# Performance work log

Measured on AMD Instinct MI355X. Metric: run time of the kernel, lower is better.

The kernel has to match this reference:

```python
import jax, jax.numpy as jnp
import numpy as np

N = 8192        # nodes (A.shape[0])
D_IN = 128      # input_dim
D_OUT = 128     # output_dim
D_THETA = 256   # hardcoded in GCN_liner_theta_1
DROP_KEEP = 0.8 # DropEdge percent


def setup_inputs() -> dict:
    key = jax.random.key(0)
    ks = jax.random.split(key, 6)
    H = jax.random.normal(ks[0], (N, D_IN), dtype=jnp.float32)
    U = jax.random.uniform(ks[1], (N, N), dtype=jnp.float32)
    upper = jnp.triu((U < 0.01).astype(jnp.float32), 1)
    A_adj = upper + upper.T + jnp.eye(N, dtype=jnp.float32)
    bn_gamma = jnp.ones((D_IN,), jnp.float32)
    bn_beta = jnp.zeros((D_IN,), jnp.float32)
    W_theta = jax.random.normal(ks[2], (D_THETA, D_IN), jnp.float32) * 0.05
    b_theta = jnp.zeros((D_THETA,), jnp.float32)
    W_out = jax.random.normal(ks[3], (D_OUT, D_IN), jnp.float32) * 0.05
    b_out = jnp.zeros((D_OUT,), jnp.float32)
    return {"H": H, "A_adj": A_adj, "bn_gamma": bn_gamma, "bn_beta": bn_beta,
            "W_theta": W_theta, "b_theta": b_theta, "W_out": W_out, "b_out": b_out}


def reference(H, A_adj, bn_gamma, bn_beta, W_theta, b_theta, W_out, b_out):
    n = H.shape[0]
    # BatchNorm1d in training mode: batch stats over the node dimension
    mean = H.mean(axis=0)
    var = H.var(axis=0)  # biased, matches torch training normalization
    Hn = (H - mean) * jax.lax.rsqrt(var + 1e-5) * bn_gamma + bn_beta

    # theta projection -> pairwise euclidean distances
    Hx = Hn @ W_theta.T + b_theta                     # [N, 256]
    sq = jnp.sum(Hx * Hx, axis=1)                     # [N]
    dist = sq[:, None] + sq[None, :] - 2.0 * (Hx @ Hx.T)
    dist = jnp.sqrt(jnp.clip(dist, 1e-12, None))      # [N, N]

    A = jnp.exp(-0.2 * dist)
    A = jnp.clip(jax.nn.sigmoid(A), 0.1, None)
    # DropEdge detaches A in the original (A never carries grad)
    A = jax.lax.stop_gradient(A)

    dkey = jax.random.key(42)
    keep = jax.random.uniform(dkey, (n, n)) < DROP_KEEP
    triu = jnp.triu(jnp.ones((n, n), dtype=bool), 0)
    Bt = jnp.where(triu & keep, A, 0.0)
    B = Bt + Bt.T - jnp.diag(jnp.diag(Bt))

    mask = jnp.ceil(A_adj * 1e-5)
    A2 = B * mask + jnp.eye(n, dtype=B.dtype)
    A3 = jnp.where(A2 > 0.6, A2, 0.0)                 # threshold (host loop in torch)

    # symmetric normalization D^-1/2 A D^-1/2 without dense diag matmuls
    d_inv_sqrt = jax.lax.rsqrt(A3.sum(axis=1))        # diag always >= 1
    A_hat = A3 * d_inv_sqrt[:, None] * d_inv_sqrt[None, :]

    out = A_hat @ (Hn @ W_out.T + b_out)              # [N, D_OUT]
    out = jnp.where(out >= 0, out, 0.01 * out)        # LeakyReLU(0.01)
    return out, A3
```

## Files before the change

kernel.cpp:

```cpp
#include <hip/hip_runtime.h>
#include <cstdint>
#include <cstddef>

#define N 8192
#define DIN 128
#define DTH 256
#define DOUT 128
#define ROWCAP 256
#define LISTCAP 256

typedef float vfloat4 __attribute__((ext_vector_type(4)));

__device__ __forceinline__ void threefry_0_42(uint32_t x0, uint32_t x1,
                                              uint32_t& o0, uint32_t& o1) {
  const uint32_t ks0 = 0u;
  const uint32_t ks1 = 42u;
  const uint32_t ks2 = 0x1BD11BDAu ^ 0u ^ 42u;
  x0 += ks0; x1 += ks1;
#define TF_R(r) { x0 += x1; x1 = (x1 << (r)) | (x1 >> (32 - (r))); x1 ^= x0; }
  TF_R(13) TF_R(15) TF_R(26) TF_R(6)
  x0 += ks1; x1 += ks2 + 1u;
  TF_R(17) TF_R(29) TF_R(16) TF_R(24)
  x0 += ks2; x1 += ks0 + 2u;
  TF_R(13) TF_R(15) TF_R(26) TF_R(6)
  x0 += ks0; x1 += ks1 + 3u;
  TF_R(17) TF_R(29) TF_R(16) TF_R(24)
  x0 += ks1; x1 += ks2 + 4u;
  TF_R(13) TF_R(15) TF_R(26) TF_R(6)
  x0 += ks2; x1 += ks0 + 5u;
#undef TF_R
  o0 = x0; o1 = x1;
}

__device__ __forceinline__ bool dropedge_keep(uint32_t t) {
  uint32_t y0, y1;
  threefry_0_42(0u, t, y0, y1);
  uint32_t bits = y0 ^ y1;
  float u = __uint_as_float((bits >> 9) | 0x3f800000u) - 1.0f;
  return u < 0.8f;
}

__device__ __forceinline__ unsigned short f2bf(float v) {
  uint32_t u = __float_as_uint(v);
  u += 0x7fffu + ((u >> 16) & 1u);
  return (unsigned short)(u >> 16);
}

__global__ __launch_bounds__(256) void k_pre(
    const float* __restrict__ H,
    const float* __restrict__ Wt, const float* __restrict__ bt,
    const float* __restrict__ Wo, const float* __restrict__ bo,
    float* __restrict__ part_s, float* __restrict__ part_s2,
    float* __restrict__ Wc, float* __restrict__ bc,
    float* __restrict__ deg ) {
  int b = blockIdx.x;
  int tid = threadIdx.x;
  if (b < 64) {
    __shared__ float ls[8][DIN];
    __shared__ float ls2[8][DIN];
    int rg = tid >> 5;
    int c4 = tid & 31;
    int rbase = b * 128;
    float s[4] = {0,0,0,0}, s2[4] = {0,0,0,0};
    for (int k = 0; k < 16; ++k) {
      int r = rbase + rg + k * 8;
      float4 h = ((const float4*)(H + (size_t)r * DIN))[c4];
      s[0] += h.x; s2[0] += h.x * h.x;
      s[1] += h.y; s2[1] += h.y * h.y;
      s[2] += h.z; s2[2] += h.z * h.z;
      s[3] += h.w; s2[3] += h.w * h.w;
    }
#pragma unroll
    for (int q = 0; q < 4; ++q) { ls[rg][c4*4+q] = s[q]; ls2[rg][c4*4+q] = s2[q]; }
    __syncthreads();
    if (tid < DIN) {
      float a = 0.f, bb = 0.f;
#pragma unroll
      for (int g = 0; g < 8; ++g) { a += ls[g][tid]; bb += ls2[g][tid]; }
      part_s[b * DIN + tid] = a;
      part_s2[b * DIN + tid] = bb;
    }
  } else if (b < 256) {
    int idx = (b - 64) * 256 + tid;
    int k = idx / 384, c = idx % 384;
    Wc[idx] = (c < 256) ? Wt[(size_t)c * DIN + k] : Wo[(size_t)(c - 256) * DIN + k];
  } else if (b < 258) {
    int c = (b - 256) * 256 + tid;
    if (c < 384) bc[c] = (c < 256) ? bt[c] : bo[c - 256];
  } else {
    int g = (b - 258) * 256 + tid;
    ((int4*)deg)[g] = make_int4(0, 0, 0, 0);
  }
}

__global__ __launch_bounds__(256) void k_rows(
    const float* __restrict__ H,
    const float* __restrict__ part_s, const float* __restrict__ part_s2,
    const float* __restrict__ gamma, const float* __restrict__ beta,
    const float* __restrict__ Wc, const float* __restrict__ bc,
    unsigned short* __restrict__ Hxh, float* __restrict__ HW,
    float* __restrict__ sq, float* __restrict__ A3) {
  int tid = threadIdx.x;
  int b = blockIdx.x;
  if (b >= 512) {
    vfloat4* row = (vfloat4*)(A3 + (size_t)(b - 512) * N);
    const vfloat4 z = {0.f, 0.f, 0.f, 0.f};
#pragma unroll
    for (int it = 0; it < 8; ++it)
      __builtin_nontemporal_store(z, row + tid + it * 256);
    return;
  }
  __shared__ __align__(16) float ssc[DIN];
  __shared__ __align__(16) float ssh[DIN];
  __shared__ float hn[16][DIN];
  if (tid < DIN) {
    float s = 0.f, s2 = 0.f;
    for (int g = 0; g < 64; ++g) { s += part_s[g*DIN+tid]; s2 += part_s2[g*DIN+tid]; }
    float mean = s * (1.0f / N);
    float var  = s2 * (1.0f / N) - mean * mean;
    float sc = rsqrtf(var + 1e-5f) * gamma[tid];
    ssc[tid] = sc;
    ssh[tid] = beta[tid] - mean * sc;
  }
  __syncthreads();
  int base = b * 16;
#pragma unroll
  for (int k = 0; k < 2; ++k) {
    int f = tid + k * 256;
    int r = f >> 5, c4 = f & 31;
    float4 h  = ((const float4*)(H + (size_t)(base + r) * DIN))[c4];
    float4 sc = ((const float4*)ssc)[c4];
    float4 sh = ((const float4*)ssh)[c4];
    h.x = h.x * sc.x + sh.x; h.y = h.y * sc.y + sh.y;
    h.z = h.z * sc.z + sh.z; h.w = h.w * sc.w + sh.w;
    ((float4*)hn[r])[c4] = h;
  }
  __syncthreads();
  int w = tid >> 6, lane = tid & 63;
  int r0 = w * 4;
  float acc[4][6];
#pragma unroll
  for (int r = 0; r < 4; ++r)
#pragma unroll
    for (int q = 0; q < 6; ++q) acc[r][q] = 0.f;

  for (int k4 = 0; k4 < 32; ++k4) {
    float4 h[4];
#pragma unroll
    for (int r = 0; r < 4; ++r) h[r] = ((const float4*)hn[r0 + r])[k4];
#pragma unroll
    for (int kk = 0; kk < 4; ++kk) {
      const float* wrow = Wc + (size_t)(k4 * 4 + kk) * 384 + lane;
      float wv[6];
#pragma unroll
      for (int q = 0; q < 6; ++q) wv[q] = wrow[64 * q];
#pragma unroll
      for (int r = 0; r < 4; ++r) {
        float hs = (kk == 0) ? h[r].x : (kk == 1) ? h[r].y
                 : (kk == 2) ? h[r].z : h[r].w;
#pragma unroll
        for (int q = 0; q < 6; ++q) acc[r][q] += hs * wv[q];
      }
    }
  }
#pragma unroll
  for (int r = 0; r < 4; ++r) {
    int row = base + r0 + r;
    float s = 0.f;
#pragma unroll
    for (int q = 0; q < 4; ++q) {
      float v = acc[r][q] + bc[lane + 64 * q];
      Hxh[(size_t)row * DTH + lane + 64 * q] = f2bf(v);
      s += v * v;
    }
#pragma unroll
    for (int off = 32; off > 0; off >>= 1) s += __shfl_xor(s, off, 64);
    if (lane == 0) sq[row] = s;
#pragma unroll
    for (int q = 4; q < 6; ++q) {
      float v = acc[r][q] + bc[lane + 64 * q];
      HW[(size_t)row * DOUT + lane + 64 * (q - 4)] = v;
    }
  }
}

__global__ __launch_bounds__(256) void k_main(
    const float* __restrict__ A_adj, const unsigned short* __restrict__ Hxh,
    const float* __restrict__ sq, float* __restrict__ A3,
    float* __restrict__ deg, int* __restrict__ nnz_cnt,
    int* __restrict__ nnz_idx, float* __restrict__ nnz_val) {
  int i = blockIdx.x;
  int tid = threadIdx.x;
  __shared__ float4 hx4[64];
  __shared__ int   s_list[LISTCAP];
  __shared__ int   s_cnt;
  if (tid == 0) s_cnt = 0;
  ((float*)hx4)[tid] = __uint_as_float(((uint32_t)Hxh[(size_t)i * DTH + tid]) << 16);
  __syncthreads();

  const vfloat4* arow = (const vfloat4*)(A_adj + (size_t)i * N);
  int q0 = i >> 2;
  for (int q4 = q0 + tid; q4 < N / 4; q4 += 256) {
    vfloat4 a = __builtin_nontemporal_load(arow + q4);
    int jb = q4 * 4;
    float av[4] = {a.x, a.y, a.z, a.w};
#pragma unroll
    for (int q = 0; q < 4; ++q) {
      int j = jb + q;
      if (av[q] != 0.f && j >= i) {
        int p = atomicAdd(&s_cnt, 1);
        if (p < LISTCAP) s_list[p] = j;
      }
    }
  }
  __syncthreads();

  int M = min(s_cnt, LISTCAP);
  float sqi = sq[i];
  for (int t = tid; t < M; t += 256) {
    int j = s_list[t];
    bool keep = dropedge_keep((uint32_t)i * (uint32_t)N + (uint32_t)j);
    float dist;
    if (j == i) {
      dist = 1e-6f;
    } else {
      const uint4* hj = (const uint4*)(Hxh + (size_t)j * DTH);
      float dot = 0.f;
#pragma unroll 8
      for (int c = 0; c < 32; ++c) {
        uint4 u = hj[c];
        float4 f0 = hx4[2 * c], f1 = hx4[2 * c + 1];
        dot += __uint_as_float(u.x << 16) * f0.x
             + __uint_as_float(u.x & 0xffff0000u) * f0.y
             + __uint_as_float(u.y << 16) * f0.z
             + __uint_as_float(u.y & 0xffff0000u) * f0.w
             + __uint_as_float(u.z << 16) * f1.x
             + __uint_as_float(u.z & 0xffff0000u) * f1.y
             + __uint_as_float(u.w << 16) * f1.z
             + __uint_as_float(u.w & 0xffff0000u) * f1.w;
      }
      dist = sqrtf(fmaxf(sqi + sq[j] - 2.0f * dot, 1e-12f));
    }
    float aval = expf(-0.2f * dist);
    float sg = fmaxf(1.0f / (1.0f + expf(-aval)), 0.1f);
    float bb = keep ? sg : 0.0f;
    float a2 = bb + ((i == j) ? 1.0f : 0.0f);
    float a3v = (a2 > 0.6f) ? a2 : 0.0f;
    if (a3v != 0.f) {
      A3[(size_t)i * N + j] = a3v;
      atomicAdd(&deg[i], a3v);
      int p = atomicAdd(&nnz_cnt[i], 1);
      if (p < ROWCAP) {
        nnz_idx[(size_t)i * ROWCAP + p] = j;
        nnz_val[(size_t)i * ROWCAP + p] = a3v;
      }
      if (j != i) {
        A3[(size_t)j * N + i] = a3v;
        atomicAdd(&deg[j], a3v);
        int p2 = atomicAdd(&nnz_cnt[j], 1);
        if (p2 < ROWCAP) {
          nnz_idx[(size_t)j * ROWCAP + p2] = i;
          nnz_val[(size_t)j * ROWCAP + p2] = a3v;
        }
      }
    }
  }
}

__global__ __launch_bounds__(128) void k_post(
    const float* __restrict__ HW, const float* __restrict__ deg,
    const int* __restrict__ nnz_cnt, const int* __restrict__ nnz_idx,
    const float* __restrict__ nnz_val, float* __restrict__ out) {
  int i = blockIdx.x;
  int c = threadIdx.x;
  int cnt = min(nnz_cnt[i], ROWCAP);
  float acc = 0.f;
  for (int e = 0; e < cnt; ++e) {
    int j = nnz_idx[(size_t)i * ROWCAP + e];
    float v = nnz_val[(size_t)i * ROWCAP + e];
    acc += v * rsqrtf(deg[j]) * HW[(size_t)j * DOUT + c];
  }
  float o = rsqrtf(deg[i]) * acc;
  out[(size_t)i * DOUT + c] = (o >= 0.f) ? o : 0.01f * o;
}

extern "C" void kernel_launch(void* const* d_in, const int* in_sizes, int n_in,
                              void* d_out, int out_size, void* d_ws, size_t ws_size,
                              hipStream_t stream) {
  const float* H     = (const float*)d_in[0];
  const float* A_adj = (const float*)d_in[1];
  const float* gamma = (const float*)d_in[2];
  const float* beta  = (const float*)d_in[3];
  const float* Wt    = (const float*)d_in[4];
  const float* bt    = (const float*)d_in[5];
  const float* Wo    = (const float*)d_in[6];
  const float* bo    = (const float*)d_in[7];

  float* out = (float*)d_out;
  float* A3  = out + (size_t)N * DOUT;

  float* ws    = (float*)d_ws;
  unsigned short* Hxh = (unsigned short*)ws;
  float* sq    = ws + (size_t)N * 128;
  float* HW    = sq + N;
  float* deg   = HW + (size_t)N * DOUT;
  int*   nnz_cnt = (int*)(deg + N);
  int*   nnz_idx = nnz_cnt + N;
  float* nnz_val = (float*)(nnz_idx + (size_t)N * ROWCAP);
  float* part_s  = nnz_val + (size_t)N * ROWCAP;
  float* part_s2 = part_s + 64 * DIN;
  float* Wc      = part_s2 + 64 * DIN;
  float* bc      = Wc + 128 * 384;

  k_pre<<<274, 256, 0, stream>>>(H, Wt, bt, Wo, bo, part_s, part_s2, Wc, bc, deg);
  k_rows<<<512 + N, 256, 0, stream>>>(H, part_s, part_s2, gamma, beta, Wc, bc,
                                      Hxh, HW, sq, A3);
  k_main<<<N, 256, 0, stream>>>(A_adj, Hxh, sq, A3, deg, nnz_cnt, nnz_idx, nnz_val);
  k_post<<<N, DOUT, 0, stream>>>(HW, deg, nnz_cnt, nnz_idx, nnz_val, out);
}
```

Measured before the change: 459.9 us.

## Build each A3 row in shared memory and write it once per block

Each block now scans its full adjacency row instead of only the upper triangle, and computes every edge from both endpoints. A symmetric DropEdge key built from min/max of the indices keeps both directions consistent. The dense A3 row is assembled in a 32KB LDS buffer and streamed out with nontemporal stores, so the separate zero-fill pass, the scattered transposed writes, and the global atomics on deg and nnz_cnt all go away. The cost is twice the distance and dot-product work and much higher LDS use per block, which may reduce occupancy.

```diff
diff --git a/kernel.cpp b/kernel.cpp
--- a/kernel.cpp
+++ b/kernel.cpp
@@ -51,8 +51,7 @@
     const float* __restrict__ Wt, const float* __restrict__ bt,
     const float* __restrict__ Wo, const float* __restrict__ bo,
     float* __restrict__ part_s, float* __restrict__ part_s2,
-    float* __restrict__ Wc, float* __restrict__ bc,
-    float* __restrict__ deg ) {
+    float* __restrict__ Wc, float* __restrict__ bc) {
   int b = blockIdx.x;
   int tid = threadIdx.x;
   if (b < 64) {
@@ -84,12 +83,9 @@
     int idx = (b - 64) * 256 + tid;
     int k = idx / 384, c = idx % 384;
     Wc[idx] = (c < 256) ? Wt[(size_t)c * DIN + k] : Wo[(size_t)(c - 256) * DIN + k];
-  } else if (b < 258) {
+  } else {
     int c = (b - 256) * 256 + tid;
     if (c < 384) bc[c] = (c < 256) ? bt[c] : bo[c - 256];
-  } else {
-    int g = (b - 258) * 256 + tid;
-    ((int4*)deg)[g] = make_int4(0, 0, 0, 0);
   }
 }
 
@@ -99,17 +95,9 @@
     const float* __restrict__ gamma, const float* __restrict__ beta,
     const float* __restrict__ Wc, const float* __restrict__ bc,
     unsigned short* __restrict__ Hxh, float* __restrict__ HW,
-    float* __restrict__ sq, float* __restrict__ A3) {
+    float* __restrict__ sq) {
   int tid = threadIdx.x;
   int b = blockIdx.x;
-  if (b >= 512) {
-    vfloat4* row = (vfloat4*)(A3 + (size_t)(b - 512) * N);
-    const vfloat4 z = {0.f, 0.f, 0.f, 0.f};
-#pragma unroll
-    for (int it = 0; it < 8; ++it)
-      __builtin_nontemporal_store(z, row + tid + it * 256);
-    return;
-  }
   __shared__ __align__(16) float ssc[DIN];
   __shared__ __align__(16) float ssh[DIN];
   __shared__ float hn[16][DIN];
@@ -191,25 +179,37 @@
     int* __restrict__ nnz_idx, float* __restrict__ nnz_val) {
   int i = blockIdx.x;
   int tid = threadIdx.x;
+  __shared__ __align__(16) float rowbuf[N];
   __shared__ float4 hx4[64];
   __shared__ int   s_list[LISTCAP];
+  __shared__ int   s_kidx[ROWCAP];
+  __shared__ float s_kval[ROWCAP];
   __shared__ int   s_cnt;
-  if (tid == 0) s_cnt = 0;
+  __shared__ int   s_keep;
+  __shared__ float s_degp[4];
+  if (tid == 0) { s_cnt = 0; s_keep = 0; }
+
+  vfloat4* rb4 = (vfloat4*)rowbuf;
+  const vfloat4 z = {0.f, 0.f, 0.f, 0.f};
+#pragma unroll
+  for (int it = 0; it < 8; ++it) rb4[tid + it * 256] = z;
   ((float*)hx4)[tid] = __uint_as_float(((uint32_t)Hxh[(size_t)i * DTH + tid]) << 16);
   __syncthreads();
 
   const vfloat4* arow = (const vfloat4*)(A_adj + (size_t)i * N);
-  int q0 = i >> 2;
-  for (int q4 = q0 + tid; q4 < N / 4; q4 += 256) {
-    vfloat4 a = __builtin_nontemporal_load(arow + q4);
-    int jb = q4 * 4;
-    float av[4] = {a.x, a.y, a.z, a.w};
+  vfloat4 av8[8];
+#pragma unroll
+  for (int it = 0; it < 8; ++it)
+    av8[it] = __builtin_nontemporal_load(arow + tid + it * 256);
+#pragma unroll
+  for (int it = 0; it < 8; ++it) {
+    int jb = (tid + it * 256) * 4;
+    float av[4] = {av8[it].x, av8[it].y, av8[it].z, av8[it].w};
 #pragma unroll
     for (int q = 0; q < 4; ++q) {
-      int j = jb + q;
-      if (av[q] != 0.f && j >= i) {
+      if (av[q] != 0.f) {
         int p = atomicAdd(&s_cnt, 1);
-        if (p < LISTCAP) s_list[p] = j;
+        if (p < LISTCAP) s_list[p] = jb + q;
       }
     }
   }
@@ -217,9 +217,9 @@
 
   int M = min(s_cnt, LISTCAP);
   float sqi = sq[i];
+  float dpart = 0.f;
   for (int t = tid; t < M; t += 256) {
     int j = s_list[t];
-    bool keep = dropedge_keep((uint32_t)i * (uint32_t)N + (uint32_t)j);
     float dist;
     if (j == i) {
       dist = 1e-6f;
@@ -241,29 +241,39 @@
       }
       dist = sqrtf(fmaxf(sqi + sq[j] - 2.0f * dot, 1e-12f));
     }
+    uint32_t uu = (uint32_t)min(i, j), vv = (uint32_t)max(i, j);
+    bool keep = dropedge_keep(uu * (uint32_t)N + vv);
     float aval = expf(-0.2f * dist);
     float sg = fmaxf(1.0f / (1.0f + expf(-aval)), 0.1f);
     float bb = keep ? sg : 0.0f;
     float a2 = bb + ((i == j) ? 1.0f : 0.0f);
     float a3v = (a2 > 0.6f) ? a2 : 0.0f;
     if (a3v != 0.f) {
-      A3[(size_t)i * N + j] = a3v;
-      atomicAdd(&deg[i], a3v);
-      int p = atomicAdd(&nnz_cnt[i], 1);
-      if (p < ROWCAP) {
-        nnz_idx[(size_t)i * ROWCAP + p] = j;
-        nnz_val[(size_t)i * ROWCAP + p] = a3v;
-      }
-      if (j != i) {
-        A3[(size_t)j * N + i] = a3v;
-        atomicAdd(&deg[j], a3v);
-        int p2 = atomicAdd(&nnz_cnt[j], 1);
-        if (p2 < ROWCAP) {
-          nnz_idx[(size_t)j * ROWCAP + p2] = i;
-          nnz_val[(size_t)j * ROWCAP + p2] = a3v;
-        }
-      }
-    }
+      rowbuf[j] = a3v;
+      dpart += a3v;
+      int p = atomicAdd(&s_keep, 1);
+      if (p < ROWCAP) { s_kidx[p] = j; s_kval[p] = a3v; }
+    }
+  }
+#pragma unroll
+  for (int off = 32; off > 0; off >>= 1) dpart += __shfl_xor(dpart, off, 64);
+  int w = tid >> 6, lane = tid & 63;
+  if (lane == 0) s_degp[w] = dpart;
+  __syncthreads();
+
+  vfloat4* orow = (vfloat4*)(A3 + (size_t)i * N);
+#pragma unroll
+  for (int it = 0; it < 8; ++it)
+    __builtin_nontemporal_store(rb4[tid + it * 256], orow + tid + it * 256);
+
+  int K = min(s_keep, ROWCAP);
+  if (tid == 0) {
+    deg[i] = s_degp[0] + s_degp[1] + s_degp[2] + s_degp[3];
+    nnz_cnt[i] = K;
+  }
+  for (int t = tid; t < K; t += 256) {
+    nnz_idx[(size_t)i * ROWCAP + t] = s_kidx[t];
+    nnz_val[(size_t)i * ROWCAP + t] = s_kval[t];
   }
 }
 
@@ -312,9 +322,9 @@
   float* Wc      = part_s2 + 64 * DIN;
   float* bc      = Wc + 128 * 384;
 
-  k_pre<<<274, 256, 0, stream>>>(H, Wt, bt, Wo, bo, part_s, part_s2, Wc, bc, deg);
-  k_rows<<<512 + N, 256, 0, stream>>>(H, part_s, part_s2, gamma, beta, Wc, bc,
-                                      Hxh, HW, sq, A3);
+  k_pre<<<258, 256, 0, stream>>>(H, Wt, bt, Wo, bo, part_s, part_s2, Wc, bc);
+  k_rows<<<512, 256, 0, stream>>>(H, part_s, part_s2, gamma, beta, Wc, bc,
+                                  Hxh, HW, sq);
   k_main<<<N, 256, 0, stream>>>(A_adj, Hxh, sq, A3, deg, nnz_cnt, nnz_idx, nnz_val);
   k_post<<<N, DOUT, 0, stream>>>(HW, deg, nnz_cnt, nnz_idx, nnz_val, out);
 }
```

Measured after the change: 506.0 us. +10.0%, slower.

## Build dense A3 rows in LDS inside the SpMM kernel instead of zero-fill plus scatter

Applied to the files above, without the earlier changes.

The separate zero-fill of the 256 MB dense A3 output and the scattered global writes from the edge kernel are removed. The final kernel now assembles each A3 row in a 32 KB shared-memory buffer from the compacted nnz list and writes it out with coalesced nontemporal stores, while also doing the aggregation with 8 edge groups per block. Per-row degree accumulation for the block's own row is reduced in-block before a single atomic. This costs large LDS use per 1024-thread block, which limits occupancy.

```diff
diff --git a/kernel.cpp b/kernel.cpp
--- a/kernel.cpp
+++ b/kernel.cpp
@@ -99,17 +99,9 @@
     const float* __restrict__ gamma, const float* __restrict__ beta,
     const float* __restrict__ Wc, const float* __restrict__ bc,
     unsigned short* __restrict__ Hxh, float* __restrict__ HW,
-    float* __restrict__ sq, float* __restrict__ A3) {
+    float* __restrict__ sq) {
   int tid = threadIdx.x;
   int b = blockIdx.x;
-  if (b >= 512) {
-    vfloat4* row = (vfloat4*)(A3 + (size_t)(b - 512) * N);
-    const vfloat4 z = {0.f, 0.f, 0.f, 0.f};
-#pragma unroll
-    for (int it = 0; it < 8; ++it)
-      __builtin_nontemporal_store(z, row + tid + it * 256);
-    return;
-  }
   __shared__ __align__(16) float ssc[DIN];
   __shared__ __align__(16) float ssh[DIN];
   __shared__ float hn[16][DIN];
@@ -184,9 +176,9 @@
   }
 }
 
-__global__ __launch_bounds__(256) void k_main(
+__global__ __launch_bounds__(256) void k_edges(
     const float* __restrict__ A_adj, const unsigned short* __restrict__ Hxh,
-    const float* __restrict__ sq, float* __restrict__ A3,
+    const float* __restrict__ sq,
     float* __restrict__ deg, int* __restrict__ nnz_cnt,
     int* __restrict__ nnz_idx, float* __restrict__ nnz_val) {
   int i = blockIdx.x;
@@ -194,6 +186,7 @@
   __shared__ float4 hx4[64];
   __shared__ int   s_list[LISTCAP];
   __shared__ int   s_cnt;
+  __shared__ float s_degp[4];
   if (tid == 0) s_cnt = 0;
   ((float*)hx4)[tid] = __uint_as_float(((uint32_t)Hxh[(size_t)i * DTH + tid]) << 16);
   __syncthreads();
@@ -217,6 +210,7 @@
 
   int M = min(s_cnt, LISTCAP);
   float sqi = sq[i];
+  float dpart = 0.f;
   for (int t = tid; t < M; t += 256) {
     int j = s_list[t];
     bool keep = dropedge_keep((uint32_t)i * (uint32_t)N + (uint32_t)j);
@@ -247,15 +241,13 @@
     float a2 = bb + ((i == j) ? 1.0f : 0.0f);
     float a3v = (a2 > 0.6f) ? a2 : 0.0f;
     if (a3v != 0.f) {
-      A3[(size_t)i * N + j] = a3v;
-      atomicAdd(&deg[i], a3v);
+      dpart += a3v;
       int p = atomicAdd(&nnz_cnt[i], 1);
       if (p < ROWCAP) {
         nnz_idx[(size_t)i * ROWCAP + p] = j;
         nnz_val[(size_t)i * ROWCAP + p] = a3v;
       }
       if (j != i) {
-        A3[(size_t)j * N + i] = a3v;
         atomicAdd(&deg[j], a3v);
         int p2 = atomicAdd(&nnz_cnt[j], 1);
         if (p2 < ROWCAP) {
@@ -265,23 +257,60 @@
       }
     }
   }
-}
-
-__global__ __launch_bounds__(128) void k_post(
+#pragma unroll
+  for (int off = 32; off > 0; off >>= 1) dpart += __shfl_xor(dpart, off, 64);
+  int w = tid >> 6, lane = tid & 63;
+  if (lane == 0) s_degp[w] = dpart;
+  __syncthreads();
+  if (tid == 0) {
+    float d = s_degp[0] + s_degp[1] + s_degp[2] + s_degp[3];
+    if (d != 0.f) atomicAdd(&deg[i], d);
+  }
+}
+
+__global__ __launch_bounds__(1024) void k_mat(
     const float* __restrict__ HW, const float* __restrict__ deg,
     const int* __restrict__ nnz_cnt, const int* __restrict__ nnz_idx,
-    const float* __restrict__ nnz_val, float* __restrict__ out) {
+    const float* __restrict__ nnz_val,
+    float* __restrict__ A3, float* __restrict__ out) {
   int i = blockIdx.x;
-  int c = threadIdx.x;
+  int tid = threadIdx.x;
+  __shared__ __align__(16) float rowbuf[N];
+  __shared__ int   s_idx[ROWCAP];
+  __shared__ float s_val[ROWCAP];
+  __shared__ float pacc[8][DOUT];
+
+  vfloat4* rb4 = (vfloat4*)rowbuf;
+  const vfloat4 z = {0.f, 0.f, 0.f, 0.f};
+  rb4[tid] = z;
+  rb4[tid + 1024] = z;
+
   int cnt = min(nnz_cnt[i], ROWCAP);
+  if (tid < cnt) {
+    s_idx[tid] = nnz_idx[(size_t)i * ROWCAP + tid];
+    s_val[tid] = nnz_val[(size_t)i * ROWCAP + tid];
+  }
+  __syncthreads();
+  if (tid < cnt) rowbuf[s_idx[tid]] = s_val[tid];
+  __syncthreads();
+
+  vfloat4* orow = (vfloat4*)(A3 + (size_t)i * N);
+  __builtin_nontemporal_store(rb4[tid], orow + tid);
+  __builtin_nontemporal_store(rb4[tid + 1024], orow + tid + 1024);
+
+  int c = tid & 127, g = tid >> 7;
   float acc = 0.f;
-  for (int e = 0; e < cnt; ++e) {
-    int j = nnz_idx[(size_t)i * ROWCAP + e];
-    float v = nnz_val[(size_t)i * ROWCAP + e];
-    acc += v * rsqrtf(deg[j]) * HW[(size_t)j * DOUT + c];
-  }
-  float o = rsqrtf(deg[i]) * acc;
-  out[(size_t)i * DOUT + c] = (o >= 0.f) ? o : 0.01f * o;
+  for (int e = g; e < cnt; e += 8)
+    acc += s_val[e] * rsqrtf(deg[s_idx[e]]) * HW[(size_t)s_idx[e] * DOUT + c];
+  pacc[g][c] = acc;
+  __syncthreads();
+  if (tid < DOUT) {
+    float a = 0.f;
+#pragma unroll
+    for (int gg = 0; gg < 8; ++gg) a += pacc[gg][tid];
+    float o = rsqrtf(deg[i]) * a;
+    out[(size_t)i * DOUT + tid] = (o >= 0.f) ? o : 0.01f * o;
+  }
 }
 
 extern "C" void kernel_launch(void* const* d_in, const int* in_sizes, int n_in,
@@ -313,8 +342,8 @@
   float* bc      = Wc + 128 * 384;
 
   k_pre<<<274, 256, 0, stream>>>(H, Wt, bt, Wo, bo, part_s, part_s2, Wc, bc, deg);
-  k_rows<<<512 + N, 256, 0, stream>>>(H, part_s, part_s2, gamma, beta, Wc, bc,
-                                      Hxh, HW, sq, A3);
-  k_main<<<N, 256, 0, stream>>>(A_adj, Hxh, sq, A3, deg, nnz_cnt, nnz_idx, nnz_val);
-  k_post<<<N, DOUT, 0, stream>>>(HW, deg, nnz_cnt, nnz_idx, nnz_val, out);
-}
+  k_rows<<<512, 256, 0, stream>>>(H, part_s, part_s2, gamma, beta, Wc, bc,
+                                  Hxh, HW, sq);
+  k_edges<<<N, 256, 0, stream>>>(A_adj, Hxh, sq, deg, nnz_cnt, nnz_idx, nnz_val);
+  k_mat<<<N, 1024, 0, stream>>>(HW, deg, nnz_cnt, nnz_idx, nnz_val, A3, out);
+}
```

Result: slower. 485.0 us (+5.5%).

## Fuse A3 zeroing into main kernel and write mirrored entries from edge lists

Applied to the files above, without the earlier changes.

Zero-filling of each A3 row moves from extra blocks in k_rows into k_main, which now owns its row before writing its upper-triangle values. The scattered transposed writes A3[j][i] are removed; k_post instead writes the lower-triangle entries from each row's nnz list while it computes the aggregation. The per-row degree atomics become a block-level reduction with a single atomic, and k_post handles four rows per 256-thread block. The aim is to cut uncoalesced global writes and atomic contention, at the cost of relying on the capped nnz lists for the lower half of A3.

```diff
diff --git a/kernel.cpp b/kernel.cpp
--- a/kernel.cpp
+++ b/kernel.cpp
@@ -99,17 +99,9 @@
     const float* __restrict__ gamma, const float* __restrict__ beta,
     const float* __restrict__ Wc, const float* __restrict__ bc,
     unsigned short* __restrict__ Hxh, float* __restrict__ HW,
-    float* __restrict__ sq, float* __restrict__ A3) {
+    float* __restrict__ sq) {
   int tid = threadIdx.x;
   int b = blockIdx.x;
-  if (b >= 512) {
-    vfloat4* row = (vfloat4*)(A3 + (size_t)(b - 512) * N);
-    const vfloat4 z = {0.f, 0.f, 0.f, 0.f};
-#pragma unroll
-    for (int it = 0; it < 8; ++it)
-      __builtin_nontemporal_store(z, row + tid + it * 256);
-    return;
-  }
   __shared__ __align__(16) float ssc[DIN];
   __shared__ __align__(16) float ssh[DIN];
   __shared__ float hn[16][DIN];
@@ -194,7 +186,15 @@
   __shared__ float4 hx4[64];
   __shared__ int   s_list[LISTCAP];
   __shared__ int   s_cnt;
+  __shared__ float s_degp[4];
   if (tid == 0) s_cnt = 0;
+
+  vfloat4* orow = (vfloat4*)(A3 + (size_t)i * N);
+  const vfloat4 z = {0.f, 0.f, 0.f, 0.f};
+#pragma unroll
+  for (int it = 0; it < 8; ++it)
+    __builtin_nontemporal_store(z, orow + tid + it * 256);
+
   ((float*)hx4)[tid] = __uint_as_float(((uint32_t)Hxh[(size_t)i * DTH + tid]) << 16);
   __syncthreads();
 
@@ -217,6 +217,7 @@
 
   int M = min(s_cnt, LISTCAP);
   float sqi = sq[i];
+  float dpart = 0.f;
   for (int t = tid; t < M; t += 256) {
     int j = s_list[t];
     bool keep = dropedge_keep((uint32_t)i * (uint32_t)N + (uint32_t)j);
@@ -248,14 +249,13 @@
     float a3v = (a2 > 0.6f) ? a2 : 0.0f;
     if (a3v != 0.f) {
       A3[(size_t)i * N + j] = a3v;
-      atomicAdd(&deg[i], a3v);
+      dpart += a3v;
       int p = atomicAdd(&nnz_cnt[i], 1);
       if (p < ROWCAP) {
         nnz_idx[(size_t)i * ROWCAP + p] = j;
         nnz_val[(size_t)i * ROWCAP + p] = a3v;
       }
       if (j != i) {
-        A3[(size_t)j * N + i] = a3v;
         atomicAdd(&deg[j], a3v);
         int p2 = atomicAdd(&nnz_cnt[j], 1);
         if (p2 < ROWCAP) {
@@ -265,23 +265,38 @@
       }
     }
   }
-}
-
-__global__ __launch_bounds__(128) void k_post(
+#pragma unroll
+  for (int off = 32; off > 0; off >>= 1) dpart += __shfl_xor(dpart, off, 64);
+  int w = tid >> 6, lane = tid & 63;
+  if (lane == 0) s_degp[w] = dpart;
+  __syncthreads();
+  if (tid == 0) {
+    float d = s_degp[0] + s_degp[1] + s_degp[2] + s_degp[3];
+    if (d != 0.f) atomicAdd(&deg[i], d);
+  }
+}
+
+__global__ __launch_bounds__(256) void k_post(
     const float* __restrict__ HW, const float* __restrict__ deg,
     const int* __restrict__ nnz_cnt, const int* __restrict__ nnz_idx,
-    const float* __restrict__ nnz_val, float* __restrict__ out) {
-  int i = blockIdx.x;
-  int c = threadIdx.x;
-  int cnt = min(nnz_cnt[i], ROWCAP);
-  float acc = 0.f;
-  for (int e = 0; e < cnt; ++e) {
-    int j = nnz_idx[(size_t)i * ROWCAP + e];
-    float v = nnz_val[(size_t)i * ROWCAP + e];
-    acc += v * rsqrtf(deg[j]) * HW[(size_t)j * DOUT + c];
-  }
-  float o = rsqrtf(deg[i]) * acc;
-  out[(size_t)i * DOUT + c] = (o >= 0.f) ? o : 0.01f * o;
+    const float* __restrict__ nnz_val,
+    float* __restrict__ A3, float* __restrict__ out) {
+  int g = threadIdx.x >> 7;
+  int c = threadIdx.x & 127;
+#pragma unroll
+  for (int k = 0; k < 2; ++k) {
+    int i = blockIdx.x * 4 + g * 2 + k;
+    int cnt = min(nnz_cnt[i], ROWCAP);
+    float acc = 0.f;
+    for (int e = 0; e < cnt; ++e) {
+      int j = nnz_idx[(size_t)i * ROWCAP + e];
+      float v = nnz_val[(size_t)i * ROWCAP + e];
+      if (c == 0 && j < i) A3[(size_t)i * N + j] = v;
+      acc += v * rsqrtf(deg[j]) * HW[(size_t)j * DOUT + c];
+    }
+    float o = rsqrtf(deg[i]) * acc;
+    out[(size_t)i * DOUT + c] = (o >= 0.f) ? o : 0.01f * o;
+  }
 }
 
 extern "C" void kernel_launch(void* const* d_in, const int* in_sizes, int n_in,
@@ -313,8 +328,8 @@
   float* bc      = Wc + 128 * 384;
 
   k_pre<<<274, 256, 0, stream>>>(H, Wt, bt, Wo, bo, part_s, part_s2, Wc, bc, deg);
-  k_rows<<<512 + N, 256, 0, stream>>>(H, part_s, part_s2, gamma, beta, Wc, bc,
-                                      Hxh, HW, sq, A3);
+  k_rows<<<512, 256, 0, stream>>>(H, part_s, part_s2, gamma, beta, Wc, bc,
+                                  Hxh, HW, sq);
   k_main<<<N, 256, 0, stream>>>(A_adj, Hxh, sq, A3, deg, nnz_cnt, nnz_idx, nnz_val);
-  k_post<<<N, DOUT, 0, stream>>>(HW, deg, nnz_cnt, nnz_idx, nnz_val, out);
-}
+  k_post<<<N / 4, 256, 0, stream>>>(HW, deg, nnz_cnt, nnz_idx, nnz_val, A3, out);
+}
```

New measurement: 481.0 us. 4.6% more time.
